# Optimization experiments

Hardware: AMD Instinct MI355X
Metric: run time of the kernel (lower is better)

The kernel has to match this reference:

```python
import jax, jax.numpy as jnp
import numpy as np
import math

WS = 7          # window size (hardcoded in RelativeSinusoidalEmbeddings)
NUM_HEADS = 12

def _rel_embeddings(ws=WS):
    # Faithful replica of RelativeSinusoidalEmbeddings.__init__
    C = 2 * ws - 1
    B = np.zeros((C, C), dtype=np.float32)
    positions = np.arange(C, dtype=np.float32)[:, None]
    divisor = np.exp(np.arange(0, C, 2, dtype=np.float32) * (-math.log(10000.0) / C))
    angles = positions * divisor
    B[:, 0::2] = np.sin(angles)
    B[:, 1::2] = np.cos(angles[:, :-1])
    x = np.arange(1.0, ws + 1.0, 1.0 / ws)                 # length ws*ws
    xi = (x[None, :] - x[:, None]).astype(np.int32)        # trunc toward zero, like torch .int()
    y = np.concatenate([np.arange(1, ws + 1)] * ws)
    yi = y[None, :] - y[:, None]
    return jnp.asarray(B[xi, yi])                           # [ws^2, ws^2]

def _shift_masks(ws=WS):
    n = ws * ws
    s = ws * (ws // 2)
    row = np.zeros((n, n), dtype=np.float32)
    row[-s:, : n - s] = -np.inf
    row[: n - s, -s:] = -np.inf
    # rearrange '(r w1) (c w2) -> (w1 r) (w2 c)'
    col = row.reshape(ws, ws, ws, ws).transpose(1, 0, 3, 2).reshape(n, n)
    return jnp.asarray(row), jnp.asarray(col)

_EMB = _rel_embeddings()
_ROW_MASK, _COL_MASK = _shift_masks()

def setup_inputs() -> dict:
    key = jax.random.key(0)
    k1, k2, k3 = jax.random.split(key, 3)
    B, H, W, D = 16, 56, 56, 384
    return {
        "x": jax.random.normal(k1, (B, H, W, D), dtype=jnp.float32),
        "w_qkv": jax.random.normal(k2, (D, 3 * D), dtype=jnp.float32) * 0.02,
        "b_qkv": jnp.zeros((3 * D,), dtype=jnp.float32),
        "w_out": jax.random.normal(k3, (D, D), dtype=jnp.float32) * 0.02,
        "b_out": jnp.zeros((D,), dtype=jnp.float32),
    }

def reference(x, w_qkv, b_qkv, w_out, b_out):
    B, Hh, Ww, d = x.shape
    ws, nh = WS, NUM_HEADS
    E = d // nh
    h, w = Hh // ws, Ww // ws
    # qkv projection, split last dim as (c, K=3) per rearrange 'b h w (c K)'
    qkv = (x @ w_qkv + b_qkv).reshape(B, Hh, Ww, d, 3)
    # mask is active since Hh != 7; shift is -ws//2 == -4 (faithful to source)
    qkv = jnp.roll(qkv, (-ws // 2, -ws // 2), axis=(1, 2))
    # 'b (h m1) (w m2) (H E) K -> b H h w (m1 m2) E K'
    qkv = qkv.reshape(B, h, ws, w, ws, nh, E, 3)
    qkv = qkv.transpose(0, 5, 1, 3, 2, 4, 6, 7).reshape(B, nh, h, w, ws * ws, E, 3)
    Q, K, V = qkv[..., 0], qkv[..., 1], qkv[..., 2]
    scores = jnp.einsum('bnhwqe,bnhwke->bnhwqk', Q, K) / math.sqrt(d / nh)
    scores = scores + _EMB
    scores = scores.at[:, :, -1, :].add(_ROW_MASK)   # last row of window grid
    scores = scores.at[:, :, :, -1].add(_COL_MASK)   # last col of window grid
    att = jax.nn.softmax(scores, axis=-1) @ V         # [B, nh, h, w, ws^2, E]
    # 'b H h w (m1 m2) E -> b (h m1) (w m2) (H E)'
    out = att.reshape(B, nh, h, w, ws, ws, E)
    out = out.transpose(0, 2, 4, 3, 5, 1, 6).reshape(B, Hh, Ww, d)
    out = jnp.roll(out, (ws // 2, ws // 2), axis=(1, 2))  # unshift by +3 (as in source)
    return out @ w_out + b_out
```

## Files before the change

kernel.cpp:

```cpp
#include <hip/hip_runtime.h>
#include <math.h>

#define DIM   384
#define NQKV  1152
#define IMG   56
#define ROWS_PER_B (IMG*IMG)

typedef unsigned short u16;
typedef unsigned int u32;
typedef __attribute__((ext_vector_type(4))) float f32x4;
typedef __attribute__((ext_vector_type(8))) short s16x8;

__device__ __forceinline__ u16 f2b(float f) {
    unsigned u = __float_as_uint(f);
    return (u16)((u + 0x7fffu + ((u >> 16) & 1u)) >> 16);
}

__device__ __forceinline__ void gl2lds16(const u16* g, u16* l) {
    __builtin_amdgcn_global_load_lds(
        (const __attribute__((address_space(1))) void*)g,
        (__attribute__((address_space(3))) void*)l, 16, 0, 0);
}

__global__ __launch_bounds__(256) void emb4_init_kernel(float* __restrict__ emb4) {
    int idx = blockIdx.x * 256 + threadIdx.x;
    if (idx >= 64 * 64) return;
    int q = idx >> 6, k = idx & 63;

    bool pad = (q >= 49) || (k >= 49);
    float base = 0.f;
    if (!pad) {
        const double step  = 1.0 / 7.0;
        const double delta = __dsub_rn(__dadd_rn(1.0, step), 1.0);
        double xk = __dadd_rn(1.0, __dmul_rn((double)k, delta));
        double xq = __dadd_rn(1.0, __dmul_rn((double)q, delta));
        int xi = (int)__dsub_rn(xk, xq);
        int yi = (k % 7) - (q % 7);
        int r = xi % 13; if (r < 0) r += 13;
        int c = yi % 13; if (c < 0) c += 13;
        const float scl = (float)(-0.7084877209212449);
        if ((c & 1) == 0) base = sinf((float)r * expf((float)c * scl));
        else              base = cosf((float)r * expf((float)(c - 1) * scl));
    }
    bool rmask = !pad && ((q >= 28) != (k >= 28));
    bool cmask = !pad && ((q % 7 >= 4) != (k % 7 >= 4));
    #pragma unroll
    for (int v = 0; v < 4; ++v) {
        float val = base;
        if (pad || ((v & 1) && rmask) || ((v & 2) && cmask)) val = -INFINITY;
        emb4[v * 4096 + idx] = val;
    }
}

__global__ __launch_bounds__(256) void cvt_f32_bf16(
    const float* __restrict__ in, u16* __restrict__ out, int n4) {
    int i = blockIdx.x * 256 + threadIdx.x;
    if (i >= n4) return;
    float4 v = ((const float4*)in)[i];
    ushort4 o;
    o.x = f2b(v.x); o.y = f2b(v.y); o.z = f2b(v.z); o.w = f2b(v.w);
    ((ushort4*)out)[i] = o;
}

__global__ __launch_bounds__(256) void cvt_transpose_bf16(
    const float* __restrict__ w, u16* __restrict__ wt, int R, int C) {
    int i = blockIdx.x * 256 + threadIdx.x;
    if (i >= R * C) return;
    int r = i / C, c = i % C;
    wt[(size_t)c * R + r] = f2b(w[i]);
}

__global__ __launch_bounds__(256) void cvt_transpose_qkv(
    const float* __restrict__ w, u16* __restrict__ wt) {
    int i = blockIdx.x * 256 + threadIdx.x;
    if (i >= 384 * 1152) return;
    int k = i / 1152, col = i % 1152;
    int ch = col / 3, comp = col % 3;
    int np = comp * 384 + ch;
    wt[(size_t)np * 384 + k] = f2b(w[i]);
}

__global__ __launch_bounds__(256) void bias_perm_kernel(
    const float* __restrict__ b, float* __restrict__ bp) {
    int n = blockIdx.x * 256 + threadIdx.x;
    if (n >= 1152) return;
    int comp = n / 384, ch = n % 384;
    bp[n] = b[ch * 3 + comp];
}

template <int MODE>
__global__ __launch_bounds__(256) void mfma_gemm(
    const u16* __restrict__ A, const u16* __restrict__ Bt,
    const float* __restrict__ bias,
    u16* __restrict__ outb, float* __restrict__ outf,
    int N, int K)
{
    __shared__ __align__(16) u16 As[3][4096];
    __shared__ __align__(16) u16 Bs[3][4096];

    const int tid  = threadIdx.x;
    const int lane = tid & 63;
    const int wid  = tid >> 6;
    const int wr   = wid >> 1, wc = wid & 1;
    const int l15  = lane & 15, l4 = lane >> 4;

    const int gx  = gridDim.x;
    const int nwg = gx * gridDim.y;
    int wg  = blockIdx.y * gx + blockIdx.x;
    int q8  = nwg >> 3, r8 = nwg & 7;
    int xcd = wg & 7, idx = wg >> 3;
    int nid = (xcd < r8 ? xcd * (q8 + 1) : r8 * (q8 + 1) + (xcd - r8) * q8) + idx;
    const int bm = nid / gx, bn = nid % gx;

    const int srow  = lane >> 2;
    const int sslot = (lane & 3) ^ ((srow >> 1) & 3);

    const u16* pA0 = A  + (size_t)(bm * 128 +      wid * 16 + srow) * K + sslot * 8;
    const u16* pA1 = A  + (size_t)(bm * 128 + 64 + wid * 16 + srow) * K + sslot * 8;
    const u16* pB0 = Bt + (size_t)(bn * 128 +      wid * 16 + srow) * K + sslot * 8;
    const u16* pB1 = Bt + (size_t)(bn * 128 + 64 + wid * 16 + srow) * K + sslot * 8;

    f32x4 acc[4][4] = {};
    const int NT = K >> 5;

    #define STAGE(t)                                                          \
        do {                                                                  \
            const int _kt = (t) << 5;                                         \
            const int _rb = (t) % 3;                                          \
            gl2lds16(pA0 + _kt, (u16*)((char*)As[_rb] + wid * 1024));         \
            gl2lds16(pA1 + _kt, (u16*)((char*)As[_rb] + 4096 + wid * 1024));  \
            gl2lds16(pB0 + _kt, (u16*)((char*)Bs[_rb] + wid * 1024));         \
            gl2lds16(pB1 + _kt, (u16*)((char*)Bs[_rb] + 4096 + wid * 1024));  \
        } while (0)

    STAGE(0);
    STAGE(1);

    for (int t = 0; t < NT; ++t) {
        if (t + 2 < NT) {
            STAGE(t + 2);
            asm volatile("s_waitcnt vmcnt(8)" ::: "memory");
        } else if (t + 2 == NT) {
            asm volatile("s_waitcnt vmcnt(4)" ::: "memory");
        } else {
            asm volatile("s_waitcnt vmcnt(0)" ::: "memory");
        }
        __builtin_amdgcn_s_barrier();
        __builtin_amdgcn_sched_barrier(0);

        const int buf = t % 3;
        s16x8 af[4], bf[4];
        #pragma unroll
        for (int m = 0; m < 4; ++m) {
            int rm = wr * 64 + m * 16 + l15;
            af[m] = *(const s16x8*)((const char*)As[buf] + rm * 64
                                    + ((l4 ^ ((rm >> 1) & 3)) << 4));
        }
        #pragma unroll
        for (int n = 0; n < 4; ++n) {
            int rn = wc * 64 + n * 16 + l15;
            bf[n] = *(const s16x8*)((const char*)Bs[buf] + rn * 64
                                    + ((l4 ^ ((rn >> 1) & 3)) << 4));
        }
        #pragma unroll
        for (int m = 0; m < 4; ++m)
            #pragma unroll
            for (int n = 0; n < 4; ++n)
                acc[m][n] = __builtin_amdgcn_mfma_f32_16x16x32_bf16(
                    af[m], bf[n], acc[m][n], 0, 0, 0);

        asm volatile("s_waitcnt lgkmcnt(0)" ::: "memory");
        __builtin_amdgcn_sched_barrier(0);
        __builtin_amdgcn_s_barrier();
    }
    #undef STAGE

    const int grow0 = bm * 128 + wr * 64;
    const int gcol0 = bn * 128 + wc * 64;
    #pragma unroll
    for (int m = 0; m < 4; ++m) {
        #pragma unroll
        for (int n = 0; n < 4; ++n) {
            int col = gcol0 + n * 16 + l15;
            float bz = bias[col];
            #pragma unroll
            for (int r = 0; r < 4; ++r) {
                int row = grow0 + m * 16 + l4 * 4 + r;
                float v = acc[m][n][r] + bz;
                if constexpr (MODE == 0)
                    outb[(size_t)row * N + col] = f2b(v);
                else
                    outf[(size_t)row * N + col] = v;
            }
        }
    }
}

__global__ __launch_bounds__(256) void attn_mfma_kernel(
    const u16* __restrict__ qkv, const float* __restrict__ emb4,
    u16* __restrict__ att)
{
    __shared__ __align__(16) u16 P4[4][64 * 72];
    __shared__ int rowIn[64];
    __shared__ int rowOut[64];

    const int tid  = threadIdx.x;
    const int lane = tid & 63;
    const int wid  = tid >> 6;
    const int l15  = lane & 15, l4 = lane >> 4;

    const int blk = blockIdx.x;
    const int hg  = blk % 3;
    const int win = (blk / 3) & 63;
    const int b   = blk / 192;
    const int bw  = win & 7, bh = win >> 3;
    const int head = hg * 4 + wid;

    if (tid < 64) {
        int pix = tid;
        int gr = (bh * 7 + pix / 7 + 4) % IMG;
        int gc = (bw * 7 + pix % 7 + 4) % IMG;
        rowIn[pix] = (b * IMG + gr) * IMG + gc;
    } else if (tid < 128) {
        int q = tid - 64;
        int fr = (bh * 7 + q / 7 + 3) % IMG;
        int fc = (bw * 7 + q % 7 + 3) % IMG;
        rowOut[q] = (b * IMG + fr) * IMG + fc;
    }
    __syncthreads();

    s16x8 qf[4], kf[4];
    #pragma unroll
    for (int n = 0; n < 4; ++n) {
        int pix = n * 16 + l15;
        size_t base = (size_t)rowIn[pix] * NQKV + head * 32 + l4 * 8;
        qf[n] = *(const s16x8*)(qkv + base);
        kf[n] = *(const s16x8*)(qkv + base + 384);
    }

    f32x4 sc[4][4] = {};
    #pragma unroll
    for (int m = 0; m < 4; ++m)
        #pragma unroll
        for (int n = 0; n < 4; ++n)
            sc[m][n] = __builtin_amdgcn_mfma_f32_16x16x32_bf16(
                kf[m], qf[n], sc[m][n], 0, 0, 0);

    const float scale = 0.17677669529663687f;
    const float* ev = emb4 + ((bh == 7 ? 1 : 0) + (bw == 7 ? 2 : 0)) * 4096;
    u16* P = P4[wid];
    u32* P32 = (u32*)P;

    #pragma unroll
    for (int n = 0; n < 4; ++n) {
        const int q = n * 16 + l15;
        float vals[4][4];
        float mx = -INFINITY;
        #pragma unroll
        for (int m = 0; m < 4; ++m) {
            float4 e4 = *(const float4*)(ev + q * 64 + m * 16 + l4 * 4);
            #pragma unroll
            for (int r = 0; r < 4; ++r) {
                float v = sc[m][n][r] * scale + ((const float*)&e4)[r];
                vals[m][r] = v;
                mx = fmaxf(mx, v);
            }
        }
        mx = fmaxf(mx, __shfl_xor(mx, 16));
        mx = fmaxf(mx, __shfl_xor(mx, 32));
        float sum = 0.f;
        #pragma unroll
        for (int m = 0; m < 4; ++m)
            #pragma unroll
            for (int r = 0; r < 4; ++r) {
                float p = __expf(vals[m][r] - mx);
                vals[m][r] = p;
                sum += p;
            }
        sum += __shfl_xor(sum, 16);
        sum += __shfl_xor(sum, 32);
        float inv = 1.f / sum;
        #pragma unroll
        for (int m = 0; m < 4; ++m) {
            u32 w0 = (u32)f2b(vals[m][0] * inv) | ((u32)f2b(vals[m][1] * inv) << 16);
            u32 w1 = (u32)f2b(vals[m][2] * inv) | ((u32)f2b(vals[m][3] * inv) << 16);
            int bidx = q * 36 + m * 8 + l4 * 2;
            P32[bidx]     = w0;
            P32[bidx + 1] = w1;
        }
    }

    f32x4 o[4][2] = {};
    #pragma unroll
    for (int kh = 0; kh < 2; ++kh) {
        s16x8 pf[4];
        #pragma unroll
        for (int mq = 0; mq < 4; ++mq)
            pf[mq] = *(const s16x8*)&P[(mq * 16 + l15) * 72 + kh * 32 + l4 * 8];
        s16x8 vf[2];
        #pragma unroll
        for (int ne = 0; ne < 2; ++ne) {
            #pragma unroll
            for (int j = 0; j < 8; ++j) {
                int pix = kh * 32 + l4 * 8 + j;
                vf[ne][j] = (short)qkv[(size_t)rowIn[pix] * NQKV + 768
                                       + head * 32 + ne * 16 + l15];
            }
        }
        #pragma unroll
        for (int mq = 0; mq < 4; ++mq)
            #pragma unroll
            for (int ne = 0; ne < 2; ++ne)
                o[mq][ne] = __builtin_amdgcn_mfma_f32_16x16x32_bf16(
                    pf[mq], vf[ne], o[mq][ne], 0, 0, 0);
    }

    #pragma unroll
    for (int mq = 0; mq < 4; ++mq) {
        #pragma unroll
        for (int r = 0; r < 4; ++r) {
            int q = mq * 16 + l4 * 4 + r;
            if (q < 49) {
                size_t rowb = (size_t)rowOut[q] * DIM + head * 32;
                #pragma unroll
                for (int ne = 0; ne < 2; ++ne)
                    att[rowb + ne * 16 + l15] = f2b(o[mq][ne][r]);
            }
        }
    }
}

extern "C" void kernel_launch(void* const* d_in, const int* in_sizes, int n_in,
                              void* d_out, int out_size, void* d_ws, size_t ws_size,
                              hipStream_t stream) {
    const float* x     = (const float*)d_in[0];
    const float* w_qkv = (const float*)d_in[1];
    const float* b_qkv = (const float*)d_in[2];
    const float* w_out = (const float*)d_in[3];
    const float* b_out = (const float*)d_in[4];
    float* out = (float*)d_out;

    char* wsp = (char*)d_ws;
    float* emb4  = (float*)wsp;
    u16*   wqkvt = (u16*)(wsp + 65536);
    u16*   woutt = (u16*)(wsp + 65536 + 884736);
    float* bqkvp = (float*)(wsp + 65536 + 884736 + 294912);
    const size_t fixed = 65536 + 884736 + 294912 + 4608;

    const size_t perb = (size_t)ROWS_PER_B * (DIM + NQKV + DIM) * 2;
    int nb = 16;
    while (nb > 2 && fixed + (size_t)nb * perb > ws_size) nb >>= 1;

    u16* xb   = (u16*)(wsp + fixed);
    u16* qkvb = xb   + (size_t)nb * ROWS_PER_B * DIM;
    u16* attb = qkvb + (size_t)nb * ROWS_PER_B * NQKV;

    emb4_init_kernel<<<16, 256, 0, stream>>>(emb4);
    cvt_transpose_qkv<<<(384 * 1152 + 255) / 256, 256, 0, stream>>>(w_qkv, wqkvt);
    cvt_transpose_bf16<<<(384 * 384 + 255) / 256, 256, 0, stream>>>(w_out, woutt, 384, 384);
    bias_perm_kernel<<<5, 256, 0, stream>>>(b_qkv, bqkvp);

    for (int b0 = 0; b0 < 16; b0 += nb) {
        const int rows = nb * ROWS_PER_B;
        const float* xa = x + (size_t)b0 * ROWS_PER_B * DIM;

        cvt_f32_bf16<<<(rows * DIM / 4 + 255) / 256, 256, 0, stream>>>(
            xa, xb, rows * DIM / 4);

        mfma_gemm<0><<<dim3(NQKV / 128, rows / 128), 256, 0, stream>>>(
            xb, wqkvt, bqkvp, qkvb, nullptr, NQKV, DIM);

        attn_mfma_kernel<<<nb * 192, 256, 0, stream>>>(qkvb, emb4, attb);

        mfma_gemm<1><<<dim3(DIM / 128, rows / 128), 256, 0, stream>>>(
            attb, woutt, b_out, nullptr, out + (size_t)b0 * ROWS_PER_B * DIM, DIM, DIM);
    }
}
```

Before: 180.9 us.

## Switch GEMM to BK=64 double-buffered tiles and raise MFMA priority in attention

The bf16 MFMA GEMM moves from a 3-stage pipeline with 32-wide K tiles to a 2-stage pipeline with 64-wide K tiles. It uses an 8-slot XOR swizzle in LDS and runs two MFMA sub-steps per barrier pair. This halves the number of barrier and wait cycles per K and makes each global-to-LDS transfer larger, at the cost of shallower prefetch. The attention kernel also wraps its MFMA blocks in s_setprio to favour matrix issue over co-resident waves.

New measurement: 179.6 us (median of 2 runs). No clear change (-0.7%).

```diff
diff --git a/kernel.cpp b/kernel.cpp
--- a/kernel.cpp
+++ b/kernel.cpp
@@ -16,7 +16,7 @@
     return (u16)((u + 0x7fffu + ((u >> 16) & 1u)) >> 16);
 }
 
-__device__ __forceinline__ void gl2lds16(const u16* g, u16* l) {
+__device__ __forceinline__ void gl2lds16(const void* g, void* l) {
     __builtin_amdgcn_global_load_lds(
         (const __attribute__((address_space(1))) void*)g,
         (__attribute__((address_space(3))) void*)l, 16, 0, 0);
@@ -95,8 +95,8 @@
     u16* __restrict__ outb, float* __restrict__ outf,
     int N, int K)
 {
-    __shared__ __align__(16) u16 As[3][4096];
-    __shared__ __align__(16) u16 Bs[3][4096];
+    __shared__ __align__(16) u16 As[2][8192];
+    __shared__ __align__(16) u16 Bs[2][8192];
 
     const int tid  = threadIdx.x;
     const int lane = tid & 63;
@@ -112,62 +112,64 @@
     int nid = (xcd < r8 ? xcd * (q8 + 1) : r8 * (q8 + 1) + (xcd - r8) * q8) + idx;
     const int bm = nid / gx, bn = nid % gx;
 
-    const int srow  = lane >> 2;
-    const int sslot = (lane & 3) ^ ((srow >> 1) & 3);
-
-    const u16* pA0 = A  + (size_t)(bm * 128 +      wid * 16 + srow) * K + sslot * 8;
-    const u16* pA1 = A  + (size_t)(bm * 128 + 64 + wid * 16 + srow) * K + sslot * 8;
-    const u16* pB0 = Bt + (size_t)(bn * 128 +      wid * 16 + srow) * K + sslot * 8;
-    const u16* pB1 = Bt + (size_t)(bn * 128 + 64 + wid * 16 + srow) * K + sslot * 8;
+    const int srow  = lane >> 3;
+    const int sslot = (lane & 7) ^ srow;
+    const u16* pA[4];
+    const u16* pB[4];
+    #pragma unroll
+    for (int i = 0; i < 4; ++i) {
+        pA[i] = A  + (size_t)(bm * 128 + wid * 32 + i * 8 + srow) * K + sslot * 8;
+        pB[i] = Bt + (size_t)(bn * 128 + wid * 32 + i * 8 + srow) * K + sslot * 8;
+    }
 
     f32x4 acc[4][4] = {};
-    const int NT = K >> 5;
-
-    #define STAGE(t)                                                          \
+    const int NT = K >> 6;
+
+    #define STAGE(t, b)                                                       \
         do {                                                                  \
-            const int _kt = (t) << 5;                                         \
-            const int _rb = (t) % 3;                                          \
-            gl2lds16(pA0 + _kt, (u16*)((char*)As[_rb] + wid * 1024));         \
-            gl2lds16(pA1 + _kt, (u16*)((char*)As[_rb] + 4096 + wid * 1024));  \
-            gl2lds16(pB0 + _kt, (u16*)((char*)Bs[_rb] + wid * 1024));         \
-            gl2lds16(pB1 + _kt, (u16*)((char*)Bs[_rb] + 4096 + wid * 1024));  \
+            const int _kt = (t) << 6;                                         \
+            _Pragma("unroll")                                                 \
+            for (int _i = 0; _i < 4; ++_i) {                                  \
+                gl2lds16(pA[_i] + _kt, &As[b][(wid * 32 + _i * 8) * 64]);     \
+                gl2lds16(pB[_i] + _kt, &Bs[b][(wid * 32 + _i * 8) * 64]);     \
+            }                                                                 \
         } while (0)
 
-    STAGE(0);
-    STAGE(1);
+    STAGE(0, 0);
 
     for (int t = 0; t < NT; ++t) {
-        if (t + 2 < NT) {
-            STAGE(t + 2);
+        const int buf = t & 1;
+        if (t + 1 < NT) {
+            STAGE(t + 1, buf ^ 1);
             asm volatile("s_waitcnt vmcnt(8)" ::: "memory");
-        } else if (t + 2 == NT) {
-            asm volatile("s_waitcnt vmcnt(4)" ::: "memory");
         } else {
             asm volatile("s_waitcnt vmcnt(0)" ::: "memory");
         }
         __builtin_amdgcn_s_barrier();
         __builtin_amdgcn_sched_barrier(0);
 
-        const int buf = t % 3;
-        s16x8 af[4], bf[4];
-        #pragma unroll
-        for (int m = 0; m < 4; ++m) {
-            int rm = wr * 64 + m * 16 + l15;
-            af[m] = *(const s16x8*)((const char*)As[buf] + rm * 64
-                                    + ((l4 ^ ((rm >> 1) & 3)) << 4));
-        }
-        #pragma unroll
-        for (int n = 0; n < 4; ++n) {
-            int rn = wc * 64 + n * 16 + l15;
-            bf[n] = *(const s16x8*)((const char*)Bs[buf] + rn * 64
-                                    + ((l4 ^ ((rn >> 1) & 3)) << 4));
-        }
-        #pragma unroll
-        for (int m = 0; m < 4; ++m)
-            #pragma unroll
-            for (int n = 0; n < 4; ++n)
-                acc[m][n] = __builtin_amdgcn_mfma_f32_16x16x32_bf16(
-                    af[m], bf[n], acc[m][n], 0, 0, 0);
+        #pragma unroll
+        for (int kk = 0; kk < 2; ++kk) {
+            s16x8 af[4], bf[4];
+            #pragma unroll
+            for (int m = 0; m < 4; ++m) {
+                int rm = wr * 64 + m * 16 + l15;
+                int sl = (kk * 4 + l4) ^ (rm & 7);
+                af[m] = *(const s16x8*)&As[buf][rm * 64 + sl * 8];
+            }
+            #pragma unroll
+            for (int n = 0; n < 4; ++n) {
+                int rn = wc * 64 + n * 16 + l15;
+                int sl = (kk * 4 + l4) ^ (rn & 7);
+                bf[n] = *(const s16x8*)&Bs[buf][rn * 64 + sl * 8];
+            }
+            #pragma unroll
+            for (int m = 0; m < 4; ++m)
+                #pragma unroll
+                for (int n = 0; n < 4; ++n)
+                    acc[m][n] = __builtin_amdgcn_mfma_f32_16x16x32_bf16(
+                        af[m], bf[n], acc[m][n], 0, 0, 0);
+        }
 
         asm volatile("s_waitcnt lgkmcnt(0)" ::: "memory");
         __builtin_amdgcn_sched_barrier(0);
@@ -239,12 +241,14 @@
     }
 
     f32x4 sc[4][4] = {};
+    __builtin_amdgcn_s_setprio(1);
     #pragma unroll
     for (int m = 0; m < 4; ++m)
         #pragma unroll
         for (int n = 0; n < 4; ++n)
             sc[m][n] = __builtin_amdgcn_mfma_f32_16x16x32_bf16(
                 kf[m], qf[n], sc[m][n], 0, 0, 0);
+    __builtin_amdgcn_s_setprio(0);
 
     const float scale = 0.17677669529663687f;
     const float* ev = emb4 + ((bh == 7 ? 1 : 0) + (bw == 7 ? 2 : 0)) * 4096;
@@ -307,12 +311,14 @@
                                        + head * 32 + ne * 16 + l15];
             }
         }
+        __builtin_amdgcn_s_setprio(1);
         #pragma unroll
         for (int mq = 0; mq < 4; ++mq)
             #pragma unroll
             for (int ne = 0; ne < 2; ++ne)
                 o[mq][ne] = __builtin_amdgcn_mfma_f32_16x16x32_bf16(
                     pf[mq], vf[ne], o[mq][ne], 0, 0, 0);
+        __builtin_amdgcn_s_setprio(0);
     }
 
     #pragma unroll
```
